# Kernel optimization log

Measured on AMD Instinct MI355X. Metric: run time of the kernel, lower is better.

The kernel has to match this reference:

```python
import jax, jax.numpy as jnp
import numpy as np

B, S, DM, H = 2, 2048, 1024, 16        # dim_model = d_model//2 = 1024
WINDOW, DILATION, N_GLOBAL = 513, 2, 32
HD = DM // H
NEG = -1e9


def build_mask(n, window_size, dilation, global_idx):
    # dilated local window: |i-j| <= (window//2)*dilation and (i-j) % dilation == 0
    i = jnp.arange(n)[:, None]
    j = jnp.arange(n)[None, :]
    d = j - i
    half = window_size // 2
    local = (jnp.abs(d) <= half * dilation) & (jnp.mod(d, dilation) == 0)
    g = jnp.zeros((n,), bool).at[global_idx].set(True)
    # symmetric global token mask: global rows and columns fully attend
    return local | g[:, None] | g[None, :]


def setup_inputs() -> dict:
    key = jax.random.key(0)
    ks = jax.random.split(key, 9)
    std = 0.02
    inp = {
        "q": jax.random.normal(ks[0], (B, S, DM), jnp.float32),
        "k": jax.random.normal(ks[1], (B, S, DM), jnp.float32),
        "v": jax.random.normal(ks[2], (B, S, DM), jnp.float32),
        "Wq": jax.random.normal(ks[3], (DM, DM), jnp.float32) * std,
        "Wk": jax.random.normal(ks[4], (DM, DM), jnp.float32) * std,
        "Wv": jax.random.normal(ks[5], (DM, DM), jnp.float32) * std,
        "Wo": jax.random.normal(ks[6], (DM, DM), jnp.float32) * std,
        "bq": jnp.zeros((DM,), jnp.float32),
        "bk": jnp.zeros((DM,), jnp.float32),
        "bv": jnp.zeros((DM,), jnp.float32),
        "bo": jnp.zeros((DM,), jnp.float32),
        "global_idx": jax.random.randint(ks[7], (N_GLOBAL,), 0, S, jnp.int64)
        if jax.config.jax_enable_x64 else jax.random.randint(ks[7], (N_GLOBAL,), 0, S, jnp.int32),
    }
    return inp


def reference(q, k, v, Wq, Wk, Wv, Wo, bq, bk, bv, bo, global_idx):
    def split(x):  # [B,S,DM] -> [B,H,S,HD]
        return x.reshape(B, S, H, HD).transpose(0, 2, 1, 3)

    qh = split(q @ Wq.T + bq)
    kh = split(k @ Wk.T + bk)
    vh = split(v @ Wv.T + bv)

    scores = jnp.einsum("bhqd,bhkd->bhqk", qh, kh) / jnp.sqrt(jnp.asarray(HD, qh.dtype))
    mask = build_mask(S, WINDOW, DILATION, global_idx)  # [S,S] bool
    scores = jnp.where(mask[None, None], scores, NEG)
    attn = jax.nn.softmax(scores, axis=-1)
    out = jnp.einsum("bhqk,bhkd->bhqd", attn, vh)
    out = out.transpose(0, 2, 1, 3).reshape(B, S, DM)
    return out @ Wo.T + bo
```

## Files before the change

kernel.cpp:

```cpp
#include <hip/hip_runtime.h>
#include <hip/hip_bf16.h>
#include <math.h>

#define BB 2
#define SS 2048
#define DMM 1024
#define HH 16
#define HDD 64
#define NGLOB 32
#define MM 4096
#define SCALE2 0.18033688f

typedef __attribute__((ext_vector_type(8))) short short8;
typedef __attribute__((ext_vector_type(4))) float float4v;

__device__ __forceinline__ short f2bf(float f) {
    union { float f; unsigned u; } x; x.f = f;
    unsigned r = (x.u + 0x7fffu + ((x.u >> 16) & 1u)) >> 16;
    return (short)r;
}

#define ASYNC16(gp, lp) __builtin_amdgcn_global_load_lds( \
    (__attribute__((address_space(1))) void*)(gp), \
    (__attribute__((address_space(3))) void*)(lp), 16, 0, 0)

#define VSL(dim, key) ((dim) * 40 + (((((key) >> 3) ^ (((dim) >> 3) & 3)) << 3) | ((key) & 7)))

__global__ void setup_globals(const int* __restrict__ gidx, int* __restrict__ g,
                              int* __restrict__ glist, int* __restrict__ gcount) {
    int t = threadIdx.x;
    for (int i = t; i < SS; i += 256) g[i] = 0;
    if (t == 0) *gcount = 0;
    __syncthreads();
    if (t < NGLOB) {
        int j = gidx[t];
        if (j >= 0 && j < SS) g[j] = 1;
    }
    __syncthreads();
    for (int j = t; j < SS; j += 256) {
        if (g[j]) {
            int p = atomicAdd(gcount, 1);
            glist[p] = j;
        }
    }
}

__global__ __launch_bounds__(256)
void convert_all(const float* __restrict__ q, const float* __restrict__ k,
                 const float* __restrict__ v,
                 const float* __restrict__ w0, const float* __restrict__ w1,
                 const float* __restrict__ w2, const float* __restrict__ w3,
                 short* __restrict__ abf, short* __restrict__ wbf) {
    int z = blockIdx.y;
    const float* src;
    short* dst;
    size_t n;
    if (z < 3) {
        src = (z == 0) ? q : (z == 1) ? k : v;
        dst = abf + (size_t)z * ((size_t)MM * DMM);
        n = (size_t)MM * DMM;
    } else {
        int y = z - 3;
        src = (y == 0) ? w0 : (y == 1) ? w1 : (y == 2) ? w2 : w3;
        dst = wbf + (size_t)y * ((size_t)DMM * DMM);
        n = (size_t)DMM * DMM;
    }
    size_t i = ((size_t)blockIdx.x * 256 + threadIdx.x) * 8;
    if (i >= n) return;
    float4 a = *(const float4*)(src + i);
    float4 b = *(const float4*)(src + i + 4);
    short8 s;
    s[0]=f2bf(a.x); s[1]=f2bf(a.y); s[2]=f2bf(a.z); s[3]=f2bf(a.w);
    s[4]=f2bf(b.x); s[5]=f2bf(b.y); s[6]=f2bf(b.z); s[7]=f2bf(b.w);
    *(short8*)(dst + i) = s;
}

template<int OBF, int HEADSPLIT>
__global__ __launch_bounds__(512, 2)
void gemm256(const short* __restrict__ Abase, const short* __restrict__ Wbase,
             const float* __restrict__ b0, const float* __restrict__ b1,
             const float* __restrict__ b2,
             void* __restrict__ O0p, void* __restrict__ O1p, void* __restrict__ O2p) {
    __shared__ short As[2][256 * 64];
    __shared__ short Ws[2][256 * 64];

    int t = threadIdx.x;
    int z = blockIdx.y;
    const short* A    = Abase + (size_t)z * ((size_t)MM * DMM);
    const short* W    = Wbase + (size_t)z * ((size_t)DMM * DMM);
    const float* bias = (z == 0) ? b0 : (z == 1) ? b1 : b2;
    void* outp        = (z == 0) ? O0p : (z == 1) ? O1p : O2p;

    int bid = blockIdx.x;
    int mt = bid & 15, nt = bid >> 4;
    int m0 = mt * 256, n0 = nt * 256;

    int lane = t & 63, w = t >> 6;
    int quad = lane >> 4, col = lane & 15;
    int wm = (w >> 2) * 128;
    int wn = (w & 3) * 64;

    float4v acc[8][4];
    #pragma unroll
    for (int i = 0; i < 8; i++)
        #pragma unroll
        for (int j = 0; j < 4; j++) acc[i][j] = (float4v){0, 0, 0, 0};

    int srow = t >> 3;
    int scol = ((t & 7) ^ (srow & 7)) * 8;
    const short* Ap = A + (size_t)(m0 + srow) * DMM + scol;
    const short* Wp = W + (size_t)(n0 + srow) * DMM + scol;

    #define STAGE256(bf, tt) do { size_t kk = (size_t)(tt) * 64; \
        ASYNC16(Ap + kk,                        &As[bf][t * 8]); \
        ASYNC16(Ap +  64 * (size_t)DMM + kk,    &As[bf][4096  + t * 8]); \
        ASYNC16(Ap + 128 * (size_t)DMM + kk,    &As[bf][8192  + t * 8]); \
        ASYNC16(Ap + 192 * (size_t)DMM + kk,    &As[bf][12288 + t * 8]); \
        ASYNC16(Wp + kk,                        &Ws[bf][t * 8]); \
        ASYNC16(Wp +  64 * (size_t)DMM + kk,    &Ws[bf][4096  + t * 8]); \
        ASYNC16(Wp + 128 * (size_t)DMM + kk,    &Ws[bf][8192  + t * 8]); \
        ASYNC16(Wp + 192 * (size_t)DMM + kk,    &Ws[bf][12288 + t * 8]); \
    } while (0)

    int c7 = col & 7;

    STAGE256(0, 0);

    for (int it = 0; it < 16; it++) {
        int cur = it & 1;
        if (it < 15) {
            STAGE256(cur ^ 1, it + 1);
            asm volatile("s_waitcnt vmcnt(8)" ::: "memory");
        } else {
            asm volatile("s_waitcnt vmcnt(0)" ::: "memory");
        }
        __builtin_amdgcn_s_barrier();

        short8 bF[4][2];
        #pragma unroll
        for (int j = 0; j < 4; j++) {
            int rB = (wn + 16 * j + col) * 64;
            #pragma unroll
            for (int ks = 0; ks < 2; ks++)
                bF[j][ks] = *(short8*)&Ws[cur][rB + ((((ks << 2) | quad) ^ c7) << 3)];
        }

        #pragma unroll
        for (int p = 0; p < 4; p++) {
            if (p) __builtin_amdgcn_s_barrier();
            short8 aF[2][2];
            #pragma unroll
            for (int u = 0; u < 2; u++) {
                int rA = (wm + 16 * (2 * p + u) + col) * 64;
                #pragma unroll
                for (int ks = 0; ks < 2; ks++)
                    aF[u][ks] = *(short8*)&As[cur][rA + ((((ks << 2) | quad) ^ c7) << 3)];
            }
            __builtin_amdgcn_s_setprio(1);
            #pragma unroll
            for (int ks = 0; ks < 2; ks++)
                #pragma unroll
                for (int u = 0; u < 2; u++)
                    #pragma unroll
                    for (int j = 0; j < 4; j++)
                        acc[2 * p + u][j] = __builtin_amdgcn_mfma_f32_16x16x32_bf16(
                            aF[u][ks], bF[j][ks], acc[2 * p + u][j], 0, 0, 0);
            __builtin_amdgcn_s_setprio(0);
        }
        __builtin_amdgcn_s_barrier();
    }
    #undef STAGE256

    #pragma unroll
    for (int i = 0; i < 8; i++) {
        #pragma unroll
        for (int j = 0; j < 4; j++) {
            int n = n0 + wn + 16 * j + col;
            float bn = bias[n];
            #pragma unroll
            for (int r = 0; r < 4; r++) {
                int m = m0 + wm + 16 * i + quad * 4 + r;
                float val = acc[i][j][r] + bn;
                size_t idx;
                if (HEADSPLIT) {
                    int b = m >> 11;
                    int s = m & 2047;
                    int h = n >> 6;
                    int hd = n & 63;
                    idx = (((size_t)b * HH + h) * SS + s) * HDD + hd;
                } else {
                    idx = (size_t)m * DMM + n;
                }
                if (OBF) ((short*)outp)[idx] = f2bf(val);
                else     ((float*)outp)[idx] = val;
            }
        }
    }
}

__global__ __launch_bounds__(256)
void gemm64p(const short* __restrict__ A, const short* __restrict__ W,
             const float* __restrict__ bias, float* __restrict__ out) {
    __shared__ short As[2][64 * 32];
    __shared__ short Ws[2][128 * 32];

    int t = threadIdx.x;
    int bid = blockIdx.x;
    int xcd = bid & 7, loc = bid >> 3;
    int nblk = loc & 7, mloc = loc >> 3;
    int m0 = (xcd * 8 + mloc) * 64;
    int n0 = nblk * 128;

    int lane = t & 63, w = t >> 6;
    int quad = lane >> 4, col = lane & 15;
    int arow0 = (w & 1) * 32;
    int ncol0 = (w >> 1) * 64;

    float4v acc[2][4];
    #pragma unroll
    for (int i = 0; i < 2; i++)
        #pragma unroll
        for (int j = 0; j < 4; j++) acc[i][j] = (float4v){0, 0, 0, 0};

    const short* Apa = A + (size_t)(m0 + (t >> 2)) * DMM + (t & 3) * 8;
    const short* Wp  = W + (size_t)(n0 + (t >> 2)) * DMM + (t & 3) * 8;

    #define STAGEW(bf, tt) do { int kk = (tt) * 32; \
        ASYNC16(Apa + kk,                     &As[bf][t * 8]); \
        ASYNC16(Wp + kk,                      &Ws[bf][t * 8]); \
        ASYNC16(Wp + 64 * (size_t)DMM + kk,   &Ws[bf][2048 + t * 8]); \
    } while (0)

    STAGEW(0, 0);
    asm volatile("s_waitcnt vmcnt(0)" ::: "memory");
    __builtin_amdgcn_s_barrier();

    for (int it = 0; it < 32; it++) {
        int cur = it & 1;
        if (it + 1 < 32) STAGEW(cur ^ 1, it + 1);

        short8 aF[2], bF[4];
        #pragma unroll
        for (int i = 0; i < 2; i++)
            aF[i] = *(short8*)&As[cur][(arow0 + 16 * i + col) * 32 + quad * 8];
        #pragma unroll
        for (int j = 0; j < 4; j++)
            bF[j] = *(short8*)&Ws[cur][(ncol0 + 16 * j + col) * 32 + quad * 8];

        __builtin_amdgcn_s_setprio(1);
        #pragma unroll
        for (int i = 0; i < 2; i++)
            #pragma unroll
            for (int j = 0; j < 4; j++)
                acc[i][j] = __builtin_amdgcn_mfma_f32_16x16x32_bf16(aF[i], bF[j], acc[i][j], 0, 0, 0);
        __builtin_amdgcn_s_setprio(0);

        asm volatile("s_waitcnt vmcnt(0)" ::: "memory");
        __builtin_amdgcn_s_barrier();
    }
    #undef STAGEW

    #pragma unroll
    for (int i = 0; i < 2; i++) {
        #pragma unroll
        for (int j = 0; j < 4; j++) {
            int n = n0 + ncol0 + 16 * j + col;
            float bn = bias[n];
            #pragma unroll
            for (int r = 0; r < 4; r++) {
                int m = m0 + arow0 + 16 * i + quad * 4 + r;
                out[(size_t)m * DMM + n] = acc[i][j][r] + bn;
            }
        }
    }
}

__global__ __launch_bounds__(256)
void band_attn(const short* __restrict__ qh, const short* __restrict__ kh,
               const short* __restrict__ vh, const int* __restrict__ glist,
               const int* __restrict__ gcount, short* __restrict__ ao) {
    __shared__ short Qs[64 * 72];
    __shared__ short Ks[32 * 72];
    __shared__ short Vt[64 * 40];
    __shared__ short Ps[4 * 16 * 40];
    __shared__ int   gjs[32];

    int t = threadIdx.x;
    int bid = blockIdx.x;
    int xcd = bid & 7, idx = bid >> 3;
    int gl  = idx >> 4;
    int qt  = idx & 15;
    int gid = xcd * 8 + gl;
    int z   = gid >> 4;
    int h   = gid & 15;
    int b = z >> 1, p = z & 1;
    int qq0 = qt * 64;
    int nG = *gcount;

    const short* Qb = qh + ((size_t)(b * HH + h) * SS) * HDD;
    const short* Kb = kh + ((size_t)(b * HH + h) * SS) * HDD;
    const short* Vb = vh + ((size_t)(b * HH + h) * SS) * HDD;

    int row8 = t >> 3;
    int dim8 = (t & 7) * 8;

    #pragma unroll
    for (int rr = 0; rr < 2; rr++) {
        int row = rr * 32 + row8;
        int i = 2 * (qq0 + row) + p;
        short8 qv = *(const short8*)(Qb + (size_t)i * HDD + dim8);
        *(short8*)&Qs[row * 72 + dim8] = qv;
    }
    if (t < 32) gjs[t] = (t < nG) ? glist[t] : -1000000;
    __syncthreads();

    int lane = t & 63, w = t >> 6;
    int quad = lane >> 4, col = lane & 15;

    short8 qf0 = *(short8*)&Qs[(16 * w + col) * 72 + quad * 8];
    short8 qf1 = *(short8*)&Qs[(16 * w + col) * 72 + 32 + quad * 8];

    float4v O0 = {0,0,0,0}, O1 = {0,0,0,0}, O2 = {0,0,0,0}, O3 = {0,0,0,0};
    float lst[4] = {0.f, 0.f, 0.f, 0.f};

    short8 kvP, vvP, kvN, vvN;
    {
        int srow = 2 * (qq0 - 256 + row8) + p;
        srow = srow < 0 ? 0 : (srow > SS - 1 ? SS - 1 : srow);
        kvP = *(const short8*)(Kb + (size_t)srow * HDD + dim8);
        vvP = *(const short8*)(Vb + (size_t)srow * HDD + dim8);
    }

    for (int c = 0; c < 19; c++) {
        __syncthreads();
        *(short8*)&Ks[row8 * 72 + dim8] = kvP;
        #pragma unroll
        for (int j = 0; j < 8; j++) {
            int d = dim8 + j;
            Vt[VSL(d, row8)] = vvP[j];
        }
        if (c < 18) {
            int cn = c + 1;
            int ch0n = qq0 - 256 + cn * 32;
            int srow;
            if (cn < 18) srow = 2 * (ch0n + row8) + p;
            else         srow = (row8 < nG) ? gjs[row8] : 0;
            srow = srow < 0 ? 0 : (srow > SS - 1 ? SS - 1 : srow);
            kvN = *(const short8*)(Kb + (size_t)srow * HDD + dim8);
            vvN = *(const short8*)(Vb + (size_t)srow * HDD + dim8);
        }
        __syncthreads();

        int ch0 = qq0 - 256 + c * 32;

        short8 kA0 = *(short8*)&Ks[col * 72 + quad * 8];
        short8 kA1 = *(short8*)&Ks[col * 72 + 32 + quad * 8];
        short8 kB0 = *(short8*)&Ks[(16 + col) * 72 + quad * 8];
        short8 kB1 = *(short8*)&Ks[(16 + col) * 72 + 32 + quad * 8];
        float4v sA = {0,0,0,0}, sB = {0,0,0,0};
        sA = __builtin_amdgcn_mfma_f32_16x16x32_bf16(qf0, kA0, sA, 0, 0, 0);
        sA = __builtin_amdgcn_mfma_f32_16x16x32_bf16(qf1, kA1, sA, 0, 0, 0);
        sB = __builtin_amdgcn_mfma_f32_16x16x32_bf16(qf0, kB0, sB, 0, 0, 0);
        sB = __builtin_amdgcn_mfma_f32_16x16x32_bf16(qf1, kB1, sB, 0, 0, 0);

        if (c < 18) {
            int nlo = -ch0;
            int nhi = 1023 - ch0;
            #pragma unroll
            for (int r = 0; r < 4; r++) {
                int qq = qq0 + 16 * w + quad * 4 + r;
                int u  = qq - ch0;
                int lo = max(u - 256, nlo);
                int hi = min(u + 256, nhi);
                bool vA = (col >= lo) && (col <= hi);
                bool vB = (col + 16 >= lo) && (col + 16 <= hi);
                float pa = vA ? exp2f(sA[r] * SCALE2) : 0.f;
                float pb = vB ? exp2f(sB[r] * SCALE2) : 0.f;
                lst[r] += pa + pb;
                Ps[(w * 16 + quad * 4 + r) * 40 + col]      = f2bf(pa);
                Ps[(w * 16 + quad * 4 + r) * 40 + col + 16] = f2bf(pb);
            }
        } else {
            #pragma unroll
            for (int r = 0; r < 4; r++) {
                int qq = qq0 + 16 * w + quad * 4 + r;
                int i = 2 * qq + p;
                int jA = gjs[col], jB = gjs[col + 16];
                int dA = jA - i, dB = jB - i;
                int aA = dA < 0 ? -dA : dA;
                int aB = dB < 0 ? -dB : dB;
                bool vA = (jA >= 0) && !((aA <= 512) && ((dA & 1) == 0));
                bool vB = (jB >= 0) && !((aB <= 512) && ((dB & 1) == 0));
                float pa = vA ? exp2f(sA[r] * SCALE2) : 0.f;
                float pb = vB ? exp2f(sB[r] * SCALE2) : 0.f;
                lst[r] += pa + pb;
                Ps[(w * 16 + quad * 4 + r) * 40 + col]      = f2bf(pa);
                Ps[(w * 16 + quad * 4 + r) * 40 + col + 16] = f2bf(pb);
            }
        }
        asm volatile("s_waitcnt lgkmcnt(0)" ::: "memory");

        short8 pf  = *(short8*)&Ps[(w * 16 + col) * 40 + quad * 8];
        short8 vf0 = *(short8*)&Vt[(col) * 40 + ((quad ^ ((col >> 3) & 3)) << 3)];
        short8 vf1 = *(short8*)&Vt[(16 + col) * 40 + ((quad ^ (((16 + col) >> 3) & 3)) << 3)];
        short8 vf2 = *(short8*)&Vt[(32 + col) * 40 + ((quad ^ (((32 + col) >> 3) & 3)) << 3)];
        short8 vf3 = *(short8*)&Vt[(48 + col) * 40 + ((quad ^ (((48 + col) >> 3) & 3)) << 3)];
        O0 = __builtin_amdgcn_mfma_f32_16x16x32_bf16(pf, vf0, O0, 0, 0, 0);
        O1 = __builtin_amdgcn_mfma_f32_16x16x32_bf16(pf, vf1, O1, 0, 0, 0);
        O2 = __builtin_amdgcn_mfma_f32_16x16x32_bf16(pf, vf2, O2, 0, 0, 0);
        O3 = __builtin_amdgcn_mfma_f32_16x16x32_bf16(pf, vf3, O3, 0, 0, 0);

        kvP = kvN; vvP = vvN;
    }

    #pragma unroll
    for (int r = 0; r < 4; r++) {
        float l = lst[r];
        #pragma unroll
        for (int mk = 1; mk < 16; mk <<= 1) l += __shfl_xor(l, mk);
        float inv = 1.0f / l;
        int q = 16 * w + quad * 4 + r;
        int i = 2 * (qq0 + q) + p;
        short* dst = ao + ((size_t)b * SS + i) * DMM + h * HDD;
        dst[col]      = f2bf(O0[r] * inv);
        dst[col + 16] = f2bf(O1[r] * inv);
        dst[col + 32] = f2bf(O2[r] * inv);
        dst[col + 48] = f2bf(O3[r] * inv);
    }
}

__global__ __launch_bounds__(256)
void global_part(const short* __restrict__ qh, const short* __restrict__ kh,
                 const short* __restrict__ vh, const int* __restrict__ glist,
                 const int* __restrict__ gcount,
                 float* __restrict__ pl, float* __restrict__ pO) {
    __shared__ short Qs[32 * 72];
    __shared__ short Ks[2][32 * 72];
    __shared__ short Vt[2][64 * 40];
    __shared__ short Ps[4 * 16 * 40];

    int t = threadIdx.x;
    int s = blockIdx.x, h = blockIdx.y, b = blockIdx.z;
    int nG = *gcount;

    const short* Qb = qh + ((size_t)(b * HH + h) * SS) * HDD;
    const short* Kb = kh + ((size_t)(b * HH + h) * SS) * HDD;
    const short* Vb = vh + ((size_t)(b * HH + h) * SS) * HDD;

    int row8 = t >> 3, dim8 = (t & 7) * 8;
    {
        int cq = row8 < nG ? row8 : 0;
        int src = glist[cq];
        short8 qv = *(const short8*)(Qb + (size_t)src * HDD + dim8);
        *(short8*)&Qs[row8 * 72 + dim8] = qv;
    }
    __syncthreads();

    int lane = t & 63, w = t >> 6;
    int quad = lane >> 4, col = lane & 15;
    int g = w >> 1, qt = w & 1;

    short8 qf0 = *(short8*)&Qs[(qt * 16 + col) * 72 + quad * 8];
    short8 qf1 = *(short8*)&Qs[(qt * 16 + col) * 72 + 32 + quad * 8];

    float4v O0 = {0,0,0,0}, O1 = {0,0,0,0}, O2 = {0,0,0,0}, O3 = {0,0,0,0};
    float lst[4] = {0.f, 0.f, 0.f, 0.f};

    int js0 = s * 256;
    for (int it = 0; it < 4; it++) {
        __syncthreads();
        int r64 = t >> 2, dimb = (t & 3) * 16;
        int j = js0 + it * 64 + r64;
        const short* kp = Kb + (size_t)j * HDD + dimb;
        const short* vp = Vb + (size_t)j * HDD + dimb;
        short8 k0 = *(const short8*)kp, k1 = *(const short8*)(kp + 8);
        short8 v0 = *(const short8*)vp, v1 = *(const short8*)(vp + 8);
        int half = r64 >> 5, r32 = r64 & 31;
        *(short8*)&Ks[half][r32 * 72 + dimb]     = k0;
        *(short8*)&Ks[half][r32 * 72 + dimb + 8] = k1;
        #pragma unroll
        for (int u = 0; u < 8; u++) {
            int d = dimb + u;
            Vt[half][VSL(d, r32)] = v0[u];
        }
        #pragma unroll
        for (int u = 0; u < 8; u++) {
            int d = dimb + 8 + u;
            Vt[half][VSL(d, r32)] = v1[u];
        }
        __syncthreads();

        short8 kA0 = *(short8*)&Ks[g][col * 72 + quad * 8];
        short8 kA1 = *(short8*)&Ks[g][col * 72 + 32 + quad * 8];
        short8 kB0 = *(short8*)&Ks[g][(16 + col) * 72 + quad * 8];
        short8 kB1 = *(short8*)&Ks[g][(16 + col) * 72 + 32 + quad * 8];
        float4v sA = {0,0,0,0}, sB = {0,0,0,0};
        sA = __builtin_amdgcn_mfma_f32_16x16x32_bf16(qf0, kA0, sA, 0, 0, 0);
        sA = __builtin_amdgcn_mfma_f32_16x16x32_bf16(qf1, kA1, sA, 0, 0, 0);
        sB = __builtin_amdgcn_mfma_f32_16x16x32_bf16(qf0, kB0, sB, 0, 0, 0);
        sB = __builtin_amdgcn_mfma_f32_16x16x32_bf16(qf1, kB1, sB, 0, 0, 0);

        #pragma unroll
        for (int r = 0; r < 4; r++) {
            float pa = exp2f(sA[r] * SCALE2);
            float pb = exp2f(sB[r] * SCALE2);
            lst[r] += pa + pb;
            Ps[(w * 16 + quad * 4 + r) * 40 + col]      = f2bf(pa);
            Ps[(w * 16 + quad * 4 + r) * 40 + col + 16] = f2bf(pb);
        }
        asm volatile("s_waitcnt lgkmcnt(0)" ::: "memory");

        short8 pf  = *(short8*)&Ps[(w * 16 + col) * 40 + quad * 8];
        short8 vf0 = *(short8*)&Vt[g][(col) * 40 + ((quad ^ ((col >> 3) & 3)) << 3)];
        short8 vf1 = *(short8*)&Vt[g][(16 + col) * 40 + ((quad ^ (((16 + col) >> 3) & 3)) << 3)];
        short8 vf2 = *(short8*)&Vt[g][(32 + col) * 40 + ((quad ^ (((32 + col) >> 3) & 3)) << 3)];
        short8 vf3 = *(short8*)&Vt[g][(48 + col) * 40 + ((quad ^ (((48 + col) >> 3) & 3)) << 3)];
        O0 = __builtin_amdgcn_mfma_f32_16x16x32_bf16(pf, vf0, O0, 0, 0, 0);
        O1 = __builtin_amdgcn_mfma_f32_16x16x32_bf16(pf, vf1, O1, 0, 0, 0);
        O2 = __builtin_amdgcn_mfma_f32_16x16x32_bf16(pf, vf2, O2, 0, 0, 0);
        O3 = __builtin_amdgcn_mfma_f32_16x16x32_bf16(pf, vf3, O3, 0, 0, 0);
    }

    int sp = s * 2 + g;
    size_t base = ((size_t)(b * HH + h) * 16 + sp) * 32;
    #pragma unroll
    for (int r = 0; r < 4; r++) {
        float l = lst[r];
        #pragma unroll
        for (int mk = 1; mk < 16; mk <<= 1) l += __shfl_xor(l, mk);
        int q = qt * 16 + quad * 4 + r;
        if (col == 0) pl[base + q] = l;
        float* Od = pO + (base + q) * 64;
        Od[col]      = O0[r];
        Od[col + 16] = O1[r];
        Od[col + 32] = O2[r];
        Od[col + 48] = O3[r];
    }
}

__global__ __launch_bounds__(256)
void global_merge(const float* __restrict__ pl, const float* __restrict__ pO,
                  const int* __restrict__ glist, const int* __restrict__ gcount,
                  short* __restrict__ ao) {
    int h = blockIdx.x, b = blockIdx.y;
    int t = threadIdx.x;
    int d = t & 63, qg = t >> 6;
    int nG = *gcount;
    size_t bh = ((size_t)(b * HH + h) * 16) * 32;

    for (int q = qg; q < nG; q += 4) {
        float L = 0.f, acc = 0.f;
        #pragma unroll
        for (int sp = 0; sp < 16; sp++) {
            L   += pl[bh + sp * 32 + q];
            acc += pO[(bh + sp * 32 + q) * 64 + d];
        }
        int i = glist[q];
        ao[((size_t)b * SS + i) * DMM + h * HDD + d] = f2bf(acc / L);
    }
}

extern "C" void kernel_launch(void* const* d_in, const int* in_sizes, int n_in,
                              void* d_out, int out_size, void* d_ws, size_t ws_size,
                              hipStream_t stream) {
    const float* q  = (const float*)d_in[0];
    const float* k  = (const float*)d_in[1];
    const float* v  = (const float*)d_in[2];
    const float* Wq = (const float*)d_in[3];
    const float* Wk = (const float*)d_in[4];
    const float* Wv = (const float*)d_in[5];
    const float* Wo = (const float*)d_in[6];
    const float* bq = (const float*)d_in[7];
    const float* bk = (const float*)d_in[8];
    const float* bv = (const float*)d_in[9];
    const float* bo = (const float*)d_in[10];
    const int* gidx = (const int*)d_in[11];
    float* out = (float*)d_out;

    const size_t NE = (size_t)BB * SS * DMM;
    const size_t WE = (size_t)DMM * DMM;
    int*   g      = (int*)d_ws;
    int*   glist  = g + SS;
    int*   gcount = glist + SS;
    short* qh     = (short*)((char*)d_ws + 32768);
    short* kh     = qh + NE;
    short* vh     = kh + NE;
    short* ao     = vh + NE;
    short* wbf    = ao + NE;
    short* wo     = wbf + 3 * WE;
    short* abf    = wbf + 4 * WE;
    float* pl     = (float*)abf;
    float* pO     = pl + 16384;

    setup_globals<<<1, 256, 0, stream>>>(gidx, g, glist, gcount);

    dim3 gc(2048, 7);
    convert_all<<<gc, 256, 0, stream>>>(q, k, v, Wq, Wk, Wv, Wo, abf, wbf);

    dim3 gq(64, 3);
    gemm256<1, 1><<<gq, 512, 0, stream>>>(abf, wbf, bq, bk, bv, qh, kh, vh);

    band_attn<<<1024, 256, 0, stream>>>(qh, kh, vh, glist, gcount, ao);

    dim3 gp(8, HH, BB);
    global_part<<<gp, 256, 0, stream>>>(qh, kh, vh, glist, gcount, pl, pO);

    dim3 gm(HH, BB);
    global_merge<<<gm, 256, 0, stream>>>(pl, pO, glist, gcount, ao);

    gemm64p<<<512, 256, 0, stream>>>(ao, wo, bo, out);
}
```

Measured before the change: 232.3 us.

## Fuse setup into convert, merge band and global attention, retile output GEMM

Three changes land together. The global-index setup kernel is folded into the conversion kernel as an extra grid row. The band-attention and global-partial kernels are merged into one launch of 1280 blocks, branched by block index. The output projection GEMM moves from 64x128 tiles with k-step 32 to 128x128 tiles with k-step 64, 512 threads, XOR-swizzled LDS and a deeper async prefetch wait. The aim is to cut launch count and tail idle time and to raise data reuse in the final GEMM, at the cost of fewer output-GEMM blocks (256) and more LDS per block.

```diff
diff --git a/kernel.cpp b/kernel.cpp
--- a/kernel.cpp
+++ b/kernel.cpp
@@ -26,32 +26,34 @@
 
 #define VSL(dim, key) ((dim) * 40 + (((((key) >> 3) ^ (((dim) >> 3) & 3)) << 3) | ((key) & 7)))
 
-__global__ void setup_globals(const int* __restrict__ gidx, int* __restrict__ g,
-                              int* __restrict__ glist, int* __restrict__ gcount) {
-    int t = threadIdx.x;
-    for (int i = t; i < SS; i += 256) g[i] = 0;
-    if (t == 0) *gcount = 0;
-    __syncthreads();
-    if (t < NGLOB) {
-        int j = gidx[t];
-        if (j >= 0 && j < SS) g[j] = 1;
-    }
-    __syncthreads();
-    for (int j = t; j < SS; j += 256) {
-        if (g[j]) {
-            int p = atomicAdd(gcount, 1);
-            glist[p] = j;
-        }
-    }
-}
-
 __global__ __launch_bounds__(256)
 void convert_all(const float* __restrict__ q, const float* __restrict__ k,
                  const float* __restrict__ v,
                  const float* __restrict__ w0, const float* __restrict__ w1,
                  const float* __restrict__ w2, const float* __restrict__ w3,
-                 short* __restrict__ abf, short* __restrict__ wbf) {
+                 short* __restrict__ abf, short* __restrict__ wbf,
+                 const int* __restrict__ gidx, int* __restrict__ g,
+                 int* __restrict__ glist, int* __restrict__ gcount) {
     int z = blockIdx.y;
+    int t = threadIdx.x;
+    if (z == 7) {
+        if (blockIdx.x != 0) return;
+        for (int i = t; i < SS; i += 256) g[i] = 0;
+        if (t == 0) *gcount = 0;
+        __syncthreads();
+        if (t < NGLOB) {
+            int j = gidx[t];
+            if (j >= 0 && j < SS) g[j] = 1;
+        }
+        __syncthreads();
+        for (int j = t; j < SS; j += 256) {
+            if (g[j]) {
+                int p = atomicAdd(gcount, 1);
+                glist[p] = j;
+            }
+        }
+        return;
+    }
     const float* src;
     short* dst;
     size_t n;
@@ -65,7 +67,7 @@
         dst = wbf + (size_t)y * ((size_t)DMM * DMM);
         n = (size_t)DMM * DMM;
     }
-    size_t i = ((size_t)blockIdx.x * 256 + threadIdx.x) * 8;
+    size_t i = ((size_t)blockIdx.x * 256 + t) * 8;
     if (i >= n) return;
     float4 a = *(const float4*)(src + i);
     float4 b = *(const float4*)(src + i + 4);
@@ -198,77 +200,98 @@
     }
 }
 
-__global__ __launch_bounds__(256)
-void gemm64p(const short* __restrict__ A, const short* __restrict__ W,
-             const float* __restrict__ bias, float* __restrict__ out) {
-    __shared__ short As[2][64 * 32];
-    __shared__ short Ws[2][128 * 32];
+__global__ __launch_bounds__(512, 2)
+void gemm128wo(const short* __restrict__ A, const short* __restrict__ W,
+               const float* __restrict__ bias, float* __restrict__ out) {
+    __shared__ short As[2][128 * 64];
+    __shared__ short Ws[2][128 * 64];
 
     int t = threadIdx.x;
     int bid = blockIdx.x;
-    int xcd = bid & 7, loc = bid >> 3;
-    int nblk = loc & 7, mloc = loc >> 3;
-    int m0 = (xcd * 8 + mloc) * 64;
-    int n0 = nblk * 128;
+    int mt = bid & 31, nt = bid >> 5;
+    int m0 = mt * 128, n0 = nt * 128;
 
     int lane = t & 63, w = t >> 6;
     int quad = lane >> 4, col = lane & 15;
-    int arow0 = (w & 1) * 32;
-    int ncol0 = (w >> 1) * 64;
-
-    float4v acc[2][4];
+    int wm = (w >> 2) * 64;
+    int wn = (w & 3) * 32;
+
+    float4v acc[4][2];
     #pragma unroll
-    for (int i = 0; i < 2; i++)
-        #pragma unroll
-        for (int j = 0; j < 4; j++) acc[i][j] = (float4v){0, 0, 0, 0};
-
-    const short* Apa = A + (size_t)(m0 + (t >> 2)) * DMM + (t & 3) * 8;
-    const short* Wp  = W + (size_t)(n0 + (t >> 2)) * DMM + (t & 3) * 8;
-
-    #define STAGEW(bf, tt) do { int kk = (tt) * 32; \
-        ASYNC16(Apa + kk,                     &As[bf][t * 8]); \
+    for (int i = 0; i < 4; i++)
+        #pragma unroll
+        for (int j = 0; j < 2; j++) acc[i][j] = (float4v){0, 0, 0, 0};
+
+    int srow = t >> 3;
+    int scol = ((t & 7) ^ (srow & 7)) * 8;
+    const short* Ap = A + (size_t)(m0 + srow) * DMM + scol;
+    const short* Wp = W + (size_t)(n0 + srow) * DMM + scol;
+
+    #define STAGEWO(bf, tt) do { size_t kk = (size_t)(tt) * 64; \
+        ASYNC16(Ap + kk,                      &As[bf][t * 8]); \
+        ASYNC16(Ap + 64 * (size_t)DMM + kk,   &As[bf][4096 + t * 8]); \
         ASYNC16(Wp + kk,                      &Ws[bf][t * 8]); \
-        ASYNC16(Wp + 64 * (size_t)DMM + kk,   &Ws[bf][2048 + t * 8]); \
+        ASYNC16(Wp + 64 * (size_t)DMM + kk,   &Ws[bf][4096 + t * 8]); \
     } while (0)
 
-    STAGEW(0, 0);
-    asm volatile("s_waitcnt vmcnt(0)" ::: "memory");
-    __builtin_amdgcn_s_barrier();
-
-    for (int it = 0; it < 32; it++) {
+    int c7 = col & 7;
+
+    STAGEWO(0, 0);
+
+    for (int it = 0; it < 16; it++) {
         int cur = it & 1;
-        if (it + 1 < 32) STAGEW(cur ^ 1, it + 1);
-
-        short8 aF[2], bF[4];
-        #pragma unroll
-        for (int i = 0; i < 2; i++)
-            aF[i] = *(short8*)&As[cur][(arow0 + 16 * i + col) * 32 + quad * 8];
-        #pragma unroll
-        for (int j = 0; j < 4; j++)
-            bF[j] = *(short8*)&Ws[cur][(ncol0 + 16 * j + col) * 32 + quad * 8];
-
-        __builtin_amdgcn_s_setprio(1);
-        #pragma unroll
-        for (int i = 0; i < 2; i++)
-            #pragma unroll
-            for (int j = 0; j < 4; j++)
-                acc[i][j] = __builtin_amdgcn_mfma_f32_16x16x32_bf16(aF[i], bF[j], acc[i][j], 0, 0, 0);
-        __builtin_amdgcn_s_setprio(0);
-
-        asm volatile("s_waitcnt vmcnt(0)" ::: "memory");
+        if (it < 15) {
+            STAGEWO(cur ^ 1, it + 1);
+            asm volatile("s_waitcnt vmcnt(4)" ::: "memory");
+        } else {
+            asm volatile("s_waitcnt vmcnt(0)" ::: "memory");
+        }
         __builtin_amdgcn_s_barrier();
-    }
-    #undef STAGEW
+
+        short8 bF[2][2];
+        #pragma unroll
+        for (int j = 0; j < 2; j++) {
+            int rB = (wn + 16 * j + col) * 64;
+            #pragma unroll
+            for (int ks = 0; ks < 2; ks++)
+                bF[j][ks] = *(short8*)&Ws[cur][rB + ((((ks << 2) | quad) ^ c7) << 3)];
+        }
+
+        #pragma unroll
+        for (int p = 0; p < 2; p++) {
+            if (p) __builtin_amdgcn_s_barrier();
+            short8 aF[2][2];
+            #pragma unroll
+            for (int u = 0; u < 2; u++) {
+                int rA = (wm + 16 * (2 * p + u) + col) * 64;
+                #pragma unroll
+                for (int ks = 0; ks < 2; ks++)
+                    aF[u][ks] = *(short8*)&As[cur][rA + ((((ks << 2) | quad) ^ c7) << 3)];
+            }
+            __builtin_amdgcn_s_setprio(1);
+            #pragma unroll
+            for (int ks = 0; ks < 2; ks++)
+                #pragma unroll
+                for (int u = 0; u < 2; u++)
+                    #pragma unroll
+                    for (int j = 0; j < 2; j++)
+                        acc[2 * p + u][j] = __builtin_amdgcn_mfma_f32_16x16x32_bf16(
+                            aF[u][ks], bF[j][ks], acc[2 * p + u][j], 0, 0, 0);
+            __builtin_amdgcn_s_setprio(0);
+        }
+        __builtin_amdgcn_s_barrier();
+    }
+    #undef STAGEWO
 
     #pragma unroll
-    for (int i = 0; i < 2; i++) {
-        #pragma unroll
-        for (int j = 0; j < 4; j++) {
-            int n = n0 + ncol0 + 16 * j + col;
+    for (int i = 0; i < 4; i++) {
+        #pragma unroll
+        for (int j = 0; j < 2; j++) {
+            int n = n0 + wn + 16 * j + col;
             float bn = bias[n];
             #pragma unroll
             for (int r = 0; r < 4; r++) {
-                int m = m0 + arow0 + 16 * i + quad * 4 + r;
+                int m = m0 + wm + 16 * i + quad * 4 + r;
                 out[(size_t)m * DMM + n] = acc[i][j][r] + bn;
             }
         }
@@ -276,265 +299,267 @@
 }
 
 __global__ __launch_bounds__(256)
-void band_attn(const short* __restrict__ qh, const short* __restrict__ kh,
-               const short* __restrict__ vh, const int* __restrict__ glist,
-               const int* __restrict__ gcount, short* __restrict__ ao) {
-    __shared__ short Qs[64 * 72];
-    __shared__ short Ks[32 * 72];
-    __shared__ short Vt[64 * 40];
-    __shared__ short Ps[4 * 16 * 40];
-    __shared__ int   gjs[32];
-
+void attn_fused(const short* __restrict__ qh, const short* __restrict__ kh,
+                const short* __restrict__ vh, const int* __restrict__ glist,
+                const int* __restrict__ gcount, short* __restrict__ ao,
+                float* __restrict__ pl, float* __restrict__ pO) {
+    __shared__ __align__(16) char smem[29184];
     int t = threadIdx.x;
     int bid = blockIdx.x;
-    int xcd = bid & 7, idx = bid >> 3;
-    int gl  = idx >> 4;
-    int qt  = idx & 15;
-    int gid = xcd * 8 + gl;
-    int z   = gid >> 4;
-    int h   = gid & 15;
-    int b = z >> 1, p = z & 1;
-    int qq0 = qt * 64;
     int nG = *gcount;
 
-    const short* Qb = qh + ((size_t)(b * HH + h) * SS) * HDD;
-    const short* Kb = kh + ((size_t)(b * HH + h) * SS) * HDD;
-    const short* Vb = vh + ((size_t)(b * HH + h) * SS) * HDD;
-
-    int row8 = t >> 3;
-    int dim8 = (t & 7) * 8;
-
-    #pragma unroll
-    for (int rr = 0; rr < 2; rr++) {
-        int row = rr * 32 + row8;
-        int i = 2 * (qq0 + row) + p;
-        short8 qv = *(const short8*)(Qb + (size_t)i * HDD + dim8);
-        *(short8*)&Qs[row * 72 + dim8] = qv;
-    }
-    if (t < 32) gjs[t] = (t < nG) ? glist[t] : -1000000;
-    __syncthreads();
-
-    int lane = t & 63, w = t >> 6;
-    int quad = lane >> 4, col = lane & 15;
-
-    short8 qf0 = *(short8*)&Qs[(16 * w + col) * 72 + quad * 8];
-    short8 qf1 = *(short8*)&Qs[(16 * w + col) * 72 + 32 + quad * 8];
-
-    float4v O0 = {0,0,0,0}, O1 = {0,0,0,0}, O2 = {0,0,0,0}, O3 = {0,0,0,0};
-    float lst[4] = {0.f, 0.f, 0.f, 0.f};
-
-    short8 kvP, vvP, kvN, vvN;
-    {
-        int srow = 2 * (qq0 - 256 + row8) + p;
-        srow = srow < 0 ? 0 : (srow > SS - 1 ? SS - 1 : srow);
-        kvP = *(const short8*)(Kb + (size_t)srow * HDD + dim8);
-        vvP = *(const short8*)(Vb + (size_t)srow * HDD + dim8);
-    }
-
-    for (int c = 0; c < 19; c++) {
+    if (bid < 1024) {
+        short* Qs = (short*)smem;
+        short* Ks = Qs + 64 * 72;
+        short* Vt = Ks + 32 * 72;
+        short* Ps = Vt + 64 * 40;
+        int*   gjs = (int*)(Ps + 4 * 16 * 40);
+
+        int xcd = bid & 7, idx = bid >> 3;
+        int gl  = idx >> 4;
+        int qt  = idx & 15;
+        int gid = xcd * 8 + gl;
+        int z   = gid >> 4;
+        int h   = gid & 15;
+        int b = z >> 1, p = z & 1;
+        int qq0 = qt * 64;
+
+        const short* Qb = qh + ((size_t)(b * HH + h) * SS) * HDD;
+        const short* Kb = kh + ((size_t)(b * HH + h) * SS) * HDD;
+        const short* Vb = vh + ((size_t)(b * HH + h) * SS) * HDD;
+
+        int row8 = t >> 3;
+        int dim8 = (t & 7) * 8;
+
+        #pragma unroll
+        for (int rr = 0; rr < 2; rr++) {
+            int row = rr * 32 + row8;
+            int i = 2 * (qq0 + row) + p;
+            short8 qv = *(const short8*)(Qb + (size_t)i * HDD + dim8);
+            *(short8*)&Qs[row * 72 + dim8] = qv;
+        }
+        if (t < 32) gjs[t] = (t < nG) ? glist[t] : -1000000;
         __syncthreads();
-        *(short8*)&Ks[row8 * 72 + dim8] = kvP;
-        #pragma unroll
-        for (int j = 0; j < 8; j++) {
-            int d = dim8 + j;
-            Vt[VSL(d, row8)] = vvP[j];
-        }
-        if (c < 18) {
-            int cn = c + 1;
-            int ch0n = qq0 - 256 + cn * 32;
-            int srow;
-            if (cn < 18) srow = 2 * (ch0n + row8) + p;
-            else         srow = (row8 < nG) ? gjs[row8] : 0;
+
+        int lane = t & 63, w = t >> 6;
+        int quad = lane >> 4, col = lane & 15;
+
+        short8 qf0 = *(short8*)&Qs[(16 * w + col) * 72 + quad * 8];
+        short8 qf1 = *(short8*)&Qs[(16 * w + col) * 72 + 32 + quad * 8];
+
+        float4v O0 = {0,0,0,0}, O1 = {0,0,0,0}, O2 = {0,0,0,0}, O3 = {0,0,0,0};
+        float lst[4] = {0.f, 0.f, 0.f, 0.f};
+
+        short8 kvP, vvP, kvN, vvN;
+        {
+            int srow = 2 * (qq0 - 256 + row8) + p;
             srow = srow < 0 ? 0 : (srow > SS - 1 ? SS - 1 : srow);
-            kvN = *(const short8*)(Kb + (size_t)srow * HDD + dim8);
-            vvN = *(const short8*)(Vb + (size_t)srow * HDD + dim8);
+            kvP = *(const short8*)(Kb + (size_t)srow * HDD + dim8);
+            vvP = *(const short8*)(Vb + (size_t)srow * HDD + dim8);
+        }
+
+        for (int c = 0; c < 19; c++) {
+            __syncthreads();
+            *(short8*)&Ks[row8 * 72 + dim8] = kvP;
+            #pragma unroll
+            for (int j = 0; j < 8; j++) {
+                int d = dim8 + j;
+                Vt[VSL(d, row8)] = vvP[j];
+            }
+            if (c < 18) {
+                int cn = c + 1;
+                int ch0n = qq0 - 256 + cn * 32;
+                int srow;
+                if (cn < 18) srow = 2 * (ch0n + row8) + p;
+                else         srow = (row8 < nG) ? gjs[row8] : 0;
+                srow = srow < 0 ? 0 : (srow > SS - 1 ? SS - 1 : srow);
+                kvN = *(const short8*)(Kb + (size_t)srow * HDD + dim8);
+                vvN = *(const short8*)(Vb + (size_t)srow * HDD + dim8);
+            }
+            __syncthreads();
+
+            int ch0 = qq0 - 256 + c * 32;
+
+            short8 kA0 = *(short8*)&Ks[col * 72 + quad * 8];
+            short8 kA1 = *(short8*)&Ks[col * 72 + 32 + quad * 8];
+            short8 kB0 = *(short8*)&Ks[(16 + col) * 72 + quad * 8];
+            short8 kB1 = *(short8*)&Ks[(16 + col) * 72 + 32 + quad * 8];
+            float4v sA = {0,0,0,0}, sB = {0,0,0,0};
+            sA = __builtin_amdgcn_mfma_f32_16x16x32_bf16(qf0, kA0, sA, 0, 0, 0);
+            sA = __builtin_amdgcn_mfma_f32_16x16x32_bf16(qf1, kA1, sA, 0, 0, 0);
+            sB = __builtin_amdgcn_mfma_f32_16x16x32_bf16(qf0, kB0, sB, 0, 0, 0);
+            sB = __builtin_amdgcn_mfma_f32_16x16x32_bf16(qf1, kB1, sB, 0, 0, 0);
+
+            if (c < 18) {
+                int nlo = -ch0;
+                int nhi = 1023 - ch0;
+                #pragma unroll
+                for (int r = 0; r < 4; r++) {
+                    int qq = qq0 + 16 * w + quad * 4 + r;
+                    int u  = qq - ch0;
+                    int lo = max(u - 256, nlo);
+                    int hi = min(u + 256, nhi);
+                    bool vA = (col >= lo) && (col <= hi);
+                    bool vB = (col + 16 >= lo) && (col + 16 <= hi);
+                    float pa = vA ? exp2f(sA[r] * SCALE2) : 0.f;
+                    float pb = vB ? exp2f(sB[r] * SCALE2) : 0.f;
+                    lst[r] += pa + pb;
+                    Ps[(w * 16 + quad * 4 + r) * 40 + col]      = f2bf(pa);
+                    Ps[(w * 16 + quad * 4 + r) * 40 + col + 16] = f2bf(pb);
+                }
+            } else {
+                #pragma unroll
+                for (int r = 0; r < 4; r++) {
+                    int qq = qq0 + 16 * w + quad * 4 + r;
+                    int i = 2 * qq + p;
+                    int jA = gjs[col], jB = gjs[col + 16];
+                    int dA = jA - i, dB = jB - i;
+                    int aA = dA < 0 ? -dA : dA;
+                    int aB = dB < 0 ? -dB : dB;
+                    bool vA = (jA >= 0) && !((aA <= 512) && ((dA & 1) == 0));
+                    bool vB = (jB >= 0) && !((aB <= 512) && ((dB & 1) == 0));
+                    float pa = vA ? exp2f(sA[r] * SCALE2) : 0.f;
+                    float pb = vB ? exp2f(sB[r] * SCALE2) : 0.f;
+                    lst[r] += pa + pb;
+                    Ps[(w * 16 + quad * 4 + r) * 40 + col]      = f2bf(pa);
+                    Ps[(w * 16 + quad * 4 + r) * 40 + col + 16] = f2bf(pb);
+                }
+            }
+            asm volatile("s_waitcnt lgkmcnt(0)" ::: "memory");
+
+            short8 pf  = *(short8*)&Ps[(w * 16 + col) * 40 + quad * 8];
+            short8 vf0 = *(short8*)&Vt[(col) * 40 + ((quad ^ ((col >> 3) & 3)) << 3)];
+            short8 vf1 = *(short8*)&Vt[(16 + col) * 40 + ((quad ^ (((16 + col) >> 3) & 3)) << 3)];
+            short8 vf2 = *(short8*)&Vt[(32 + col) * 40 + ((quad ^ (((32 + col) >> 3) & 3)) << 3)];
+            short8 vf3 = *(short8*)&Vt[(48 + col) * 40 + ((quad ^ (((48 + col) >> 3) & 3)) << 3)];
+            O0 = __builtin_amdgcn_mfma_f32_16x16x32_bf16(pf, vf0, O0, 0, 0, 0);
+            O1 = __builtin_amdgcn_mfma_f32_16x16x32_bf16(pf, vf1, O1, 0, 0, 0);
+            O2 = __builtin_amdgcn_mfma_f32_16x16x32_bf16(pf, vf2, O2, 0, 0, 0);
+            O3 = __builtin_amdgcn_mfma_f32_16x16x32_bf16(pf, vf3, O3, 0, 0, 0);
+
+            kvP = kvN; vvP = vvN;
+        }
+
+        #pragma unroll
+        for (int r = 0; r < 4; r++) {
+            float l = lst[r];
+            #pragma unroll
+            for (int mk = 1; mk < 16; mk <<= 1) l += __shfl_xor(l, mk);
+            float inv = 1.0f / l;
+            int q = 16 * w + quad * 4 + r;
+            int i = 2 * (qq0 + q) + p;
+            short* dst = ao + ((size_t)b * SS + i) * DMM + h * HDD;
+            dst[col]      = f2bf(O0[r] * inv);
+            dst[col + 16] = f2bf(O1[r] * inv);
+            dst[col + 32] = f2bf(O2[r] * inv);
+            dst[col + 48] = f2bf(O3[r] * inv);
+        }
+    } else {
+        short* Qs  = (short*)smem;
+        short* Ksf = Qs + 32 * 72;
+        short* Vtf = Ksf + 2 * 32 * 72;
+        short* Ps  = Vtf + 2 * 64 * 40;
+
+        int r0 = bid - 1024;
+        int s = r0 & 7, h = (r0 >> 3) & 15, b = r0 >> 7;
+
+        const short* Qb = qh + ((size_t)(b * HH + h) * SS) * HDD;
+        const short* Kb = kh + ((size_t)(b * HH + h) * SS) * HDD;
+        const short* Vb = vh + ((size_t)(b * HH + h) * SS) * HDD;
+
+        int row8 = t >> 3, dim8 = (t & 7) * 8;
+        {
+            int cq = row8 < nG ? row8 : 0;
+            int src = glist[cq];
+            short8 qv = *(const short8*)(Qb + (size_t)src * HDD + dim8);
+            *(short8*)&Qs[row8 * 72 + dim8] = qv;
         }
         __syncthreads();
 
-        int ch0 = qq0 - 256 + c * 32;
-
-        short8 kA0 = *(short8*)&Ks[col * 72 + quad * 8];
-        short8 kA1 = *(short8*)&Ks[col * 72 + 32 + quad * 8];
-        short8 kB0 = *(short8*)&Ks[(16 + col) * 72 + quad * 8];
-        short8 kB1 = *(short8*)&Ks[(16 + col) * 72 + 32 + quad * 8];
-        float4v sA = {0,0,0,0}, sB = {0,0,0,0};
-        sA = __builtin_amdgcn_mfma_f32_16x16x32_bf16(qf0, kA0, sA, 0, 0, 0);
-        sA = __builtin_amdgcn_mfma_f32_16x16x32_bf16(qf1, kA1, sA, 0, 0, 0);
-        sB = __builtin_amdgcn_mfma_f32_16x16x32_bf16(qf0, kB0, sB, 0, 0, 0);
-        sB = __builtin_amdgcn_mfma_f32_16x16x32_bf16(qf1, kB1, sB, 0, 0, 0);
-
-        if (c < 18) {
-            int nlo = -ch0;
-            int nhi = 1023 - ch0;
+        int lane = t & 63, w = t >> 6;
+        int quad = lane >> 4, col = lane & 15;
+        int g = w >> 1, qt = w & 1;
+
+        short8 qf0 = *(short8*)&Qs[(qt * 16 + col) * 72 + quad * 8];
+        short8 qf1 = *(short8*)&Qs[(qt * 16 + col) * 72 + 32 + quad * 8];
+
+        float4v O0 = {0,0,0,0}, O1 = {0,0,0,0}, O2 = {0,0,0,0}, O3 = {0,0,0,0};
+        float lst[4] = {0.f, 0.f, 0.f, 0.f};
+
+        int js0 = s * 256;
+        for (int it = 0; it < 4; it++) {
+            __syncthreads();
+            int r64 = t >> 2, dimb = (t & 3) * 16;
+            int j = js0 + it * 64 + r64;
+            const short* kp = Kb + (size_t)j * HDD + dimb;
+            const short* vp = Vb + (size_t)j * HDD + dimb;
+            short8 k0 = *(const short8*)kp, k1 = *(const short8*)(kp + 8);
+            short8 v0 = *(const short8*)vp, v1 = *(const short8*)(vp + 8);
+            int half = r64 >> 5, r32 = r64 & 31;
+            short* Ksh = Ksf + half * (32 * 72);
+            short* Vth = Vtf + half * (64 * 40);
+            *(short8*)&Ksh[r32 * 72 + dimb]     = k0;
+            *(short8*)&Ksh[r32 * 72 + dimb + 8] = k1;
+            #pragma unroll
+            for (int u = 0; u < 8; u++) {
+                int d = dimb + u;
+                Vth[VSL(d, r32)] = v0[u];
+            }
+            #pragma unroll
+            for (int u = 0; u < 8; u++) {
+                int d = dimb + 8 + u;
+                Vth[VSL(d, r32)] = v1[u];
+            }
+            __syncthreads();
+
+            short* Ksg = Ksf + g * (32 * 72);
+            short* Vtg = Vtf + g * (64 * 40);
+            short8 kA0 = *(short8*)&Ksg[col * 72 + quad * 8];
+            short8 kA1 = *(short8*)&Ksg[col * 72 + 32 + quad * 8];
+            short8 kB0 = *(short8*)&Ksg[(16 + col) * 72 + quad * 8];
+            short8 kB1 = *(short8*)&Ksg[(16 + col) * 72 + 32 + quad * 8];
+            float4v sA = {0,0,0,0}, sB = {0,0,0,0};
+            sA = __builtin_amdgcn_mfma_f32_16x16x32_bf16(qf0, kA0, sA, 0, 0, 0);
+            sA = __builtin_amdgcn_mfma_f32_16x16x32_bf16(qf1, kA1, sA, 0, 0, 0);
+            sB = __builtin_amdgcn_mfma_f32_16x16x32_bf16(qf0, kB0, sB, 0, 0, 0);
+            sB = __builtin_amdgcn_mfma_f32_16x16x32_bf16(qf1, kB1, sB, 0, 0, 0);
+
             #pragma unroll
             for (int r = 0; r < 4; r++) {
-                int qq = qq0 + 16 * w + quad * 4 + r;
-                int u  = qq - ch0;
-                int lo = max(u - 256, nlo);
-                int hi = min(u + 256, nhi);
-                bool vA = (col >= lo) && (col <= hi);
-                bool vB = (col + 16 >= lo) && (col + 16 <= hi);
-                float pa = vA ? exp2f(sA[r] * SCALE2) : 0.f;
-                float pb = vB ? exp2f(sB[r] * SCALE2) : 0.f;
+                float pa = exp2f(sA[r] * SCALE2);
+                float pb = exp2f(sB[r] * SCALE2);
                 lst[r] += pa + pb;
                 Ps[(w * 16 + quad * 4 + r) * 40 + col]      = f2bf(pa);
                 Ps[(w * 16 + quad * 4 + r) * 40 + col + 16] = f2bf(pb);
             }
-        } else {
-            #pragma unroll
-            for (int r = 0; r < 4; r++) {
-                int qq = qq0 + 16 * w + quad * 4 + r;
-                int i = 2 * qq + p;
-                int jA = gjs[col], jB = gjs[col + 16];
-                int dA = jA - i, dB = jB - i;
-                int aA = dA < 0 ? -dA : dA;
-                int aB = dB < 0 ? -dB : dB;
-                bool vA = (jA >= 0) && !((aA <= 512) && ((dA & 1) == 0));
-                bool vB = (jB >= 0) && !((aB <= 512) && ((dB & 1) == 0));
-                float pa = vA ? exp2f(sA[r] * SCALE2) : 0.f;
-                float pb = vB ? exp2f(sB[r] * SCALE2) : 0.f;
-                lst[r] += pa + pb;
-                Ps[(w * 16 + quad * 4 + r) * 40 + col]      = f2bf(pa);
-                Ps[(w * 16 + quad * 4 + r) * 40 + col + 16] = f2bf(pb);
-            }
-        }
-        asm volatile("s_waitcnt lgkmcnt(0)" ::: "memory");
-
-        short8 pf  = *(short8*)&Ps[(w * 16 + col) * 40 + quad * 8];
-        short8 vf0 = *(short8*)&Vt[(col) * 40 + ((quad ^ ((col >> 3) & 3)) << 3)];
-        short8 vf1 = *(short8*)&Vt[(16 + col) * 40 + ((quad ^ (((16 + col) >> 3) & 3)) << 3)];
-        short8 vf2 = *(short8*)&Vt[(32 + col) * 40 + ((quad ^ (((32 + col) >> 3) & 3)) << 3)];
-        short8 vf3 = *(short8*)&Vt[(48 + col) * 40 + ((quad ^ (((48 + col) >> 3) & 3)) << 3)];
-        O0 = __builtin_amdgcn_mfma_f32_16x16x32_bf16(pf, vf0, O0, 0, 0, 0);
-        O1 = __builtin_amdgcn_mfma_f32_16x16x32_bf16(pf, vf1, O1, 0, 0, 0);
-        O2 = __builtin_amdgcn_mfma_f32_16x16x32_bf16(pf, vf2, O2, 0, 0, 0);
-        O3 = __builtin_amdgcn_mfma_f32_16x16x32_bf16(pf, vf3, O3, 0, 0, 0);
-
-        kvP = kvN; vvP = vvN;
-    }
-
-    #pragma unroll
-    for (int r = 0; r < 4; r++) {
-        float l = lst[r];
-        #pragma unroll
-        for (int mk = 1; mk < 16; mk <<= 1) l += __shfl_xor(l, mk);
-        float inv = 1.0f / l;
-        int q = 16 * w + quad * 4 + r;
-        int i = 2 * (qq0 + q) + p;
-        short* dst = ao + ((size_t)b * SS + i) * DMM + h * HDD;
-        dst[col]      = f2bf(O0[r] * inv);
-        dst[col + 16] = f2bf(O1[r] * inv);
-        dst[col + 32] = f2bf(O2[r] * inv);
-        dst[col + 48] = f2bf(O3[r] * inv);
-    }
-}
-
-__global__ __launch_bounds__(256)
-void global_part(const short* __restrict__ qh, const short* __restrict__ kh,
-                 const short* __restrict__ vh, const int* __restrict__ glist,
-                 const int* __restrict__ gcount,
-                 float* __restrict__ pl, float* __restrict__ pO) {
-    __shared__ short Qs[32 * 72];
-    __shared__ short Ks[2][32 * 72];
-    __shared__ short Vt[2][64 * 40];
-    __shared__ short Ps[4 * 16 * 40];
-
-    int t = threadIdx.x;
-    int s = blockIdx.x, h = blockIdx.y, b = blockIdx.z;
-    int nG = *gcount;
-
-    const short* Qb = qh + ((size_t)(b * HH + h) * SS) * HDD;
-    const short* Kb = kh + ((size_t)(b * HH + h) * SS) * HDD;
-    const short* Vb = vh + ((size_t)(b * HH + h) * SS) * HDD;
-
-    int row8 = t >> 3, dim8 = (t & 7) * 8;
-    {
-        int cq = row8 < nG ? row8 : 0;
-        int src = glist[cq];
-        short8 qv = *(const short8*)(Qb + (size_t)src * HDD + dim8);
-        *(short8*)&Qs[row8 * 72 + dim8] = qv;
-    }
-    __syncthreads();
-
-    int lane = t & 63, w = t >> 6;
-    int quad = lane >> 4, col = lane & 15;
-    int g = w >> 1, qt = w & 1;
-
-    short8 qf0 = *(short8*)&Qs[(qt * 16 + col) * 72 + quad * 8];
-    short8 qf1 = *(short8*)&Qs[(qt * 16 + col) * 72 + 32 + quad * 8];
-
-    float4v O0 = {0,0,0,0}, O1 = {0,0,0,0}, O2 = {0,0,0,0}, O3 = {0,0,0,0};
-    float lst[4] = {0.f, 0.f, 0.f, 0.f};
-
-    int js0 = s * 256;
-    for (int it = 0; it < 4; it++) {
-        __syncthreads();
-        int r64 = t >> 2, dimb = (t & 3) * 16;
-        int j = js0 + it * 64 + r64;
-        const short* kp = Kb + (size_t)j * HDD + dimb;
-        const short* vp = Vb + (size_t)j * HDD + dimb;
-        short8 k0 = *(const short8*)kp, k1 = *(const short8*)(kp + 8);
-        short8 v0 = *(const short8*)vp, v1 = *(const short8*)(vp + 8);
-        int half = r64 >> 5, r32 = r64 & 31;
-        *(short8*)&Ks[half][r32 * 72 + dimb]     = k0;
-        *(short8*)&Ks[half][r32 * 72 + dimb + 8] = k1;
-        #pragma unroll
-        for (int u = 0; u < 8; u++) {
-            int d = dimb + u;
-            Vt[half][VSL(d, r32)] = v0[u];
-        }
-        #pragma unroll
-        for (int u = 0; u < 8; u++) {
-            int d = dimb + 8 + u;
-            Vt[half][VSL(d, r32)] = v1[u];
-        }
-        __syncthreads();
-
-        short8 kA0 = *(short8*)&Ks[g][col * 72 + quad * 8];
-        short8 kA1 = *(short8*)&Ks[g][col * 72 + 32 + quad * 8];
-        short8 kB0 = *(short8*)&Ks[g][(16 + col) * 72 + quad * 8];
-        short8 kB1 = *(short8*)&Ks[g][(16 + col) * 72 + 32 + quad * 8];
-        float4v sA = {0,0,0,0}, sB = {0,0,0,0};
-        sA = __builtin_amdgcn_mfma_f32_16x16x32_bf16(qf0, kA0, sA, 0, 0, 0);
-        sA = __builtin_amdgcn_mfma_f32_16x16x32_bf16(qf1, kA1, sA, 0, 0, 0);
-        sB = __builtin_amdgcn_mfma_f32_16x16x32_bf16(qf0, kB0, sB, 0, 0, 0);
-        sB = __builtin_amdgcn_mfma_f32_16x16x32_bf16(qf1, kB1, sB, 0, 0, 0);
-
+            asm volatile("s_waitcnt lgkmcnt(0)" ::: "memory");
+
+            short8 pf  = *(short8*)&Ps[(w * 16 + col) * 40 + quad * 8];
+            short8 vf0 = *(short8*)&Vtg[(col) * 40 + ((quad ^ ((col >> 3) & 3)) << 3)];
+            short8 vf1 = *(short8*)&Vtg[(16 + col) * 40 + ((quad ^ (((16 + col) >> 3) & 3)) << 3)];
+            short8 vf2 = *(short8*)&Vtg[(32 + col) * 40 + ((quad ^ (((32 + col) >> 3) & 3)) << 3)];
+            short8 vf3 = *(short8*)&Vtg[(48 + col) * 40 + ((quad ^ (((48 + col) >> 3) & 3)) << 3)];
+            O0 = __builtin_amdgcn_mfma_f32_16x16x32_bf16(pf, vf0, O0, 0, 0, 0);
+            O1 = __builtin_amdgcn_mfma_f32_16x16x32_bf16(pf, vf1, O1, 0, 0, 0);
+            O2 = __builtin_amdgcn_mfma_f32_16x16x32_bf16(pf, vf2, O2, 0, 0, 0);
+            O3 = __builtin_amdgcn_mfma_f32_16x16x32_bf16(pf, vf3, O3, 0, 0, 0);
+        }
+
+        int sp = s * 2 + g;
+        size_t base = ((size_t)(b * HH + h) * 16 + sp) * 32;
         #pragma unroll
         for (int r = 0; r < 4; r++) {
-            float pa = exp2f(sA[r] * SCALE2);
-            float pb = exp2f(sB[r] * SCALE2);
-            lst[r] += pa + pb;
-            Ps[(w * 16 + quad * 4 + r) * 40 + col]      = f2bf(pa);
-            Ps[(w * 16 + quad * 4 + r) * 40 + col + 16] = f2bf(pb);
-        }
-        asm volatile("s_waitcnt lgkmcnt(0)" ::: "memory");
-
-        short8 pf  = *(short8*)&Ps[(w * 16 + col) * 40 + quad * 8];
-        short8 vf0 = *(short8*)&Vt[g][(col) * 40 + ((quad ^ ((col >> 3) & 3)) << 3)];
-        short8 vf1 = *(short8*)&Vt[g][(16 + col) * 40 + ((quad ^ (((16 + col) >> 3) & 3)) << 3)];
-        short8 vf2 = *(short8*)&Vt[g][(32 + col) * 40 + ((quad ^ (((32 + col) >> 3) & 3)) << 3)];
-        short8 vf3 = *(short8*)&Vt[g][(48 + col) * 40 + ((quad ^ (((48 + col) >> 3) & 3)) << 3)];
-        O0 = __builtin_amdgcn_mfma_f32_16x16x32_bf16(pf, vf0, O0, 0, 0, 0);
-        O1 = __builtin_amdgcn_mfma_f32_16x16x32_bf16(pf, vf1, O1, 0, 0, 0);
-        O2 = __builtin_amdgcn_mfma_f32_16x16x32_bf16(pf, vf2, O2, 0, 0, 0);
-        O3 = __builtin_amdgcn_mfma_f32_16x16x32_bf16(pf, vf3, O3, 0, 0, 0);
-    }
-
-    int sp = s * 2 + g;
-    size_t base = ((size_t)(b * HH + h) * 16 + sp) * 32;
-    #pragma unroll
-    for (int r = 0; r < 4; r++) {
-        float l = lst[r];
-        #pragma unroll
-        for (int mk = 1; mk < 16; mk <<= 1) l += __shfl_xor(l, mk);
-        int q = qt * 16 + quad * 4 + r;
-        if (col == 0) pl[base + q] = l;
-        float* Od = pO + (base + q) * 64;
-        Od[col]      = O0[r];
-        Od[col + 16] = O1[r];
-        Od[col + 32] = O2[r];
-        Od[col + 48] = O3[r];
+            float l = lst[r];
+            #pragma unroll
+            for (int mk = 1; mk < 16; mk <<= 1) l += __shfl_xor(l, mk);
+            int q = qt * 16 + quad * 4 + r;
+            if (col == 0) pl[base + q] = l;
+            float* Od = pO + (base + q) * 64;
+            Od[col]      = O0[r];
+            Od[col + 16] = O1[r];
+            Od[col + 32] = O2[r];
+            Od[col + 48] = O3[r];
+        }
     }
 }
 
@@ -592,21 +617,17 @@
     float* pl     = (float*)abf;
     float* pO     = pl + 16384;
 
-    setup_globals<<<1, 256, 0, stream>>>(gidx, g, glist, gcount);
-
-    dim3 gc(2048, 7);
-    convert_all<<<gc, 256, 0, stream>>>(q, k, v, Wq, Wk, Wv, Wo, abf, wbf);
+    dim3 gc(2048, 8);
+    convert_all<<<gc, 256, 0, stream>>>(q, k, v, Wq, Wk, Wv, Wo, abf, wbf,
+                                        gidx, g, glist, gcount);
 
     dim3 gq(64, 3);
     gemm256<1, 1><<<gq, 512, 0, stream>>>(abf, wbf, bq, bk, bv, qh, kh, vh);
 
-    band_attn<<<1024, 256, 0, stream>>>(qh, kh, vh, glist, gcount, ao);
-
-    dim3 gp(8, HH, BB);
-    global_part<<<gp, 256, 0, stream>>>(qh, kh, vh, glist, gcount, pl, pO);
+    attn_fused<<<1280, 256, 0, stream>>>(qh, kh, vh, glist, gcount, ao, pl, pO);
 
     dim3 gm(HH, BB);
     global_merge<<<gm, 256, 0, stream>>>(pl, pO, glist, gcount, ao);
 
-    gemm64p<<<512, 256, 0, stream>>>(ao, wo, bo, out);
+    gemm128wo<<<256, 512, 0, stream>>>(ao, wo, bo, out);
 }
```

After: 215.6 us. -7.2%, faster.
